# Kernel tuning notes

Hardware: AMD Instinct MI355X
Metric: run time of the kernel (lower is better)

Reference implementation:

```python
import jax, jax.numpy as jnp
import numpy as np

N = 30000      # nodes
E = 480000     # edges
H = 128        # hidden_nf
NQ = 7         # qubits
D = 2 ** NQ    # 128, quantum state dim == embedding_size
NL = 2         # block n_layers (QGCL layers)
QL = 2         # quantum circuit layers inside each QGCL
NORM = 100.0   # normalization_factor ('sum' aggregation)
NORM_CONST = 1.0


def _cnot_perm_indices(n):
    # Composed permutation for CNOT(0,1)...CNOT(n-2,n-1), CNOT(n-1,0).
    # PennyLane convention: wire 0 is the most significant bit.
    idx = np.arange(2 ** n)
    pairs = [(i, i + 1) for i in range(n - 1)] + [(n - 1, 0)]
    g = None
    for c, t in pairs:
        cb = (idx >> (n - 1 - c)) & 1
        f = idx ^ (cb << (n - 1 - t))  # flip target bit if control set (involution)
        g = f if g is None else g[f]
    return g

_CNOT_G = jnp.asarray(_cnot_perm_indices(NQ))


def _quantum_states(q_in, coeffs, A_re, A_im):
    """Vectorized VQC over all nodes. q_in [N,D] real -> [N,D] complex state."""
    norm = jnp.sqrt(jnp.sum(q_in ** 2, axis=1, keepdims=True) + 1e-12)
    s = (q_in / norm).astype(jnp.complex64)  # normalized initial state per node
    I = jnp.eye(D, dtype=jnp.complex64)
    for j in range(QL):
        # Cayley transform -> unitary
        A = (A_re[j] + 1j * A_im[j]).astype(jnp.complex64)
        A = A + A.conj().T
        q = (A - 1j * I) @ jnp.linalg.inv(A + 1j * I)
        # single-qubit layer: RY(b) @ RX(a) on every qubit -> kron power
        a, b = coeffs[j, 0].astype(jnp.complex64), coeffs[j, 1].astype(jnp.complex64)
        ca, sa = jnp.cos(a / 2), jnp.sin(a / 2)
        cb, sb = jnp.cos(b / 2), jnp.sin(b / 2)
        RX = jnp.stack([jnp.stack([ca, -1j * sa]), jnp.stack([-1j * sa, ca])])
        RY = jnp.stack([jnp.stack([cb, -sb]), jnp.stack([sb, cb])])
        G = RY @ RX
        Gk = G
        for _ in range(NQ - 1):
            Gk = jnp.kron(Gk, G)
        s = s @ q.T            # QubitUnitary
        s = s @ Gk.T           # RX/RY on all qubits
        s = s[:, _CNOT_G]      # CNOT ring (pure permutation)
    return s


def setup_inputs() -> dict:
    key = jax.random.key(0)
    ks = jax.random.split(key, 20)
    return {
        "h": jax.random.normal(ks[0], (N, H), jnp.float32),
        "x": jax.random.normal(ks[1], (N, 3), jnp.float32),
        "edge_index": jax.random.randint(ks[2], (2, E), 0, N, jnp.int32),
        "edge_attr": jax.random.normal(ks[3], (E, 1), jnp.float32),
        "e_w1": jax.random.normal(ks[4], (NL, 2 * H + 2, H), jnp.float32) * 0.05,
        "e_b1": jnp.zeros((NL, H), jnp.float32),
        "e_w2": jax.random.normal(ks[5], (NL, H, H), jnp.float32) * 0.05,
        "e_b2": jnp.zeros((NL, H), jnp.float32),
        "enc_w": jax.random.normal(ks[6], (NL, 2 * H, D), jnp.float32) * 0.05,
        "enc_b": jnp.zeros((NL, D), jnp.float32),
        "coeffs": jax.random.normal(ks[7], (NL, QL, 2), jnp.float32) * 0.1,
        "A_re": jax.random.normal(ks[8], (NL, QL, D, D), jnp.float32) * 0.01,
        "A_im": jax.random.normal(ks[9], (NL, QL, D, D), jnp.float32) * 0.01,
        "dec_w": jax.random.normal(ks[10], (NL, D, H), jnp.float32) * 0.05,
        "dec_b": jnp.zeros((NL, H), jnp.float32),
        "c_w1": jax.random.normal(ks[11], (2 * H + 2, H), jnp.float32) * 0.05,
        "c_b1": jnp.zeros((H,), jnp.float32),
        "c_w2": jax.random.normal(ks[12], (H, H), jnp.float32) * 0.05,
        "c_b2": jnp.zeros((H,), jnp.float32),
        "c_w3": jax.random.normal(ks[13], (H, 1), jnp.float32) * 0.001,  # xavier gain=0.001
    }


def reference(h, x, edge_index, edge_attr, e_w1, e_b1, e_w2, e_b2, enc_w, enc_b,
              coeffs, A_re, A_im, dec_w, dec_b, c_w1, c_b1, c_w2, c_b2, c_w3):
    row, col = edge_index[0], edge_index[1]
    # coord2diff
    diff = x[row] - x[col]
    radial = jnp.sum(diff ** 2, axis=1, keepdims=True)     # [E,1] (used as 'distances')
    coord_diff = diff / (jnp.sqrt(radial + 1e-8) + NORM_CONST)
    eattr = jnp.concatenate([radial, edge_attr], axis=1)   # [E,2]

    for l in range(NL):  # QGCL layers
        m = jnp.concatenate([h[row], h[col], eattr], axis=1)       # [E, 2H+2]
        m = jax.nn.silu(m @ e_w1[l] + e_b1[l])
        m = jax.nn.silu(m @ e_w2[l] + e_b2[l])                     # edge messages mij
        agg = jax.ops.segment_sum(m, row, num_segments=N) / NORM   # scatter-add
        q_in = jnp.concatenate([h, agg], axis=1) @ enc_w[l] + enc_b[l]
        # quantum part is detached in the original (torch .detach + re-tensor)
        qs = jax.lax.stop_gradient(
            _quantum_states(q_in, coeffs[l], A_re[l], A_im[l]))
        h = h + qs.real.astype(h.dtype) @ dec_w[l] + dec_b[l]

    # EquivariantUpdate (tanh=False)
    t = jnp.concatenate([h[row], h[col], eattr], axis=1)
    t = jax.nn.silu(t @ c_w1 + c_b1)
    t = jax.nn.silu(t @ c_w2 + c_b2)
    t = t @ c_w3                                                   # [E,1]
    trans = coord_diff * t
    x = x + jax.ops.segment_sum(trans, row, num_segments=N) / NORM
    return h, x
```

## Files before the change

kernel.cpp:

```cpp
#include <hip/hip_runtime.h>
#include <math.h>

#define N_NODES 30000
#define N_EDGES 480000
#define HDIM 128
#define EPB 64
#define AS 296
#define NAS 264
#define MS 136

typedef __attribute__((ext_vector_type(8))) short short8b;
typedef __attribute__((ext_vector_type(4))) float f32x4;

__device__ __forceinline__ float silu_f(float v) {
  return v / (1.0f + __expf(-v));
}

__device__ __forceinline__ unsigned short f2bf(float f) {
  unsigned int u = __float_as_uint(f);
  unsigned int r = u + 0x7fffu + ((u >> 16) & 1u);
  return (unsigned short)(r >> 16);
}

__global__ void init_out_kernel(const float* __restrict__ h,
                                const float* __restrict__ x,
                                float* __restrict__ out) {
  int idx = blockIdx.x * 256 + threadIdx.x;
  out[idx] = h[idx];
  if (idx < N_NODES * 3) out[N_NODES * HDIM + idx] = x[idx];
}

__global__ void h_to_bf_kernel(const float* __restrict__ h,
                               ushort* __restrict__ hbf) {
  int idx = blockIdx.x * 256 + threadIdx.x;
  float4 v = ((const float4*)h)[idx];
  ushort4 o;
  o.x = f2bf(v.x); o.y = f2bf(v.y); o.z = f2bf(v.z); o.w = f2bf(v.w);
  ((ushort4*)hbf)[idx] = o;
}

__global__ void convert_w_kernel(const float* __restrict__ W,
                                 ushort* __restrict__ dst, int Kreal, int KT) {
  int idx = blockIdx.x * 256 + threadIdx.x;
  if (idx >= KT * 4096) return;
  int kt = idx >> 12, rem = idx & 4095, n = rem >> 5, kk = rem & 31;
  int k = kt * 32 + kk;
  float v = (k < Kreal) ? W[(size_t)k * HDIM + n] : 0.0f;
  dst[idx] = f2bf(v);
}

__global__ void count_kernel(const int* __restrict__ ei, int* __restrict__ cursor) {
  int e = blockIdx.x * 256 + threadIdx.x;
  atomicAdd(&cursor[ei[e]], 1);
}

__global__ __launch_bounds__(1024) void scan_kernel(int* __restrict__ cursor,
                                                    int* __restrict__ cstart) {
  __shared__ int sums[1024];
  const int tid = threadIdx.x;
  const int base = tid * 30;
  int local[30];
  int s = 0;
#pragma unroll
  for (int j = 0; j < 30; ++j) {
    int idx = base + j;
    int d = (idx < N_NODES) ? cursor[idx] : 0;
    local[j] = s;
    s += d;
  }
  sums[tid] = s;
  __syncthreads();
  for (int off = 1; off < 1024; off <<= 1) {
    int add = (tid >= off) ? sums[tid - off] : 0;
    __syncthreads();
    sums[tid] += add;
    __syncthreads();
  }
  int excl = (tid == 0) ? 0 : sums[tid - 1];
#pragma unroll
  for (int j = 0; j < 30; ++j) {
    int idx = base + j;
    if (idx < N_NODES) {
      int v = excl + local[j];
      cursor[idx] = v;
      cstart[idx] = v;
    }
  }
}

__global__ void fill_kernel(const int* __restrict__ ei, int* __restrict__ cursor,
                            int* __restrict__ elist) {
  int e = blockIdx.x * 256 + threadIdx.x;
  int r = ei[e];
  int pos = atomicAdd(&cursor[r], 1);
  elist[pos] = e;
}

__global__ void perm_kernel(int* __restrict__ g) {
  int i = threadIdx.x;
  int v = i;
  const int cs[7] = {6, 5, 4, 3, 2, 1, 0};
  const int ts[7] = {0, 6, 5, 4, 3, 2, 1};
#pragma unroll
  for (int p = 0; p < 7; ++p) {
    int cb = (v >> (6 - cs[p])) & 1;
    v = v ^ (cb << (6 - ts[p]));
  }
  g[i] = v;
}

__global__ void ns_init_kernel(const float* __restrict__ Are,
                               const float* __restrict__ Aim,
                               float2* __restrict__ X) {
  int lj = blockIdx.y;
  int idx = blockIdx.x * 256 + threadIdx.x;
  int r = idx >> 7, c = idx & 127;
  const float* are = Are + (size_t)lj * 16384;
  const float* aim = Aim + (size_t)lj * 16384;
  float re = are[r * 128 + c] + are[c * 128 + r];
  float im = aim[r * 128 + c] - aim[c * 128 + r];
  if (r == c) im -= 1.0f;
  X[(size_t)lj * 16384 + idx] = make_float2(re, im);
}

__global__ void ns_bx_kernel(const float* __restrict__ Are,
                             const float* __restrict__ Aim,
                             const float2* __restrict__ X,
                             float2* __restrict__ T) {
  int lj = blockIdx.y;
  int idx = blockIdx.x * 256 + threadIdx.x;
  int r = idx >> 7, c = idx & 127;
  const float* are = Are + (size_t)lj * 16384;
  const float* aim = Aim + (size_t)lj * 16384;
  const float2* x = X + (size_t)lj * 16384;
  float2 acc = make_float2(0.f, 0.f);
  for (int k = 0; k < 128; ++k) {
    float re = are[r * 128 + k] + are[k * 128 + r];
    float im = aim[r * 128 + k] - aim[k * 128 + r];
    if (k == r) im += 1.0f;
    float2 b = x[k * 128 + c];
    acc.x += re * b.x - im * b.y;
    acc.y += re * b.y + im * b.x;
  }
  T[(size_t)lj * 16384 + idx] = acc;
}

__global__ void ns_upd_kernel(const float2* __restrict__ X,
                              const float2* __restrict__ T,
                              float2* __restrict__ Xn) {
  int lj = blockIdx.y;
  int idx = blockIdx.x * 256 + threadIdx.x;
  int r = idx >> 7, c = idx & 127;
  const float2* x = X + (size_t)lj * 16384;
  const float2* t = T + (size_t)lj * 16384;
  float2 acc = make_float2(0.f, 0.f);
  for (int k = 0; k < 128; ++k) {
    float2 a = x[r * 128 + k];
    float2 b = t[k * 128 + c];
    acc.x += a.x * b.x - a.y * b.y;
    acc.y += a.x * b.y + a.y * b.x;
  }
  float2 xc = x[r * 128 + c];
  Xn[(size_t)lj * 16384 + idx] = make_float2(2.f * xc.x - acc.x, 2.f * xc.y - acc.y);
}

__global__ void qmat_kernel(const float* __restrict__ Are,
                            const float* __restrict__ Aim,
                            const float2* __restrict__ binvg,
                            float2* __restrict__ qm) {
  int lj = blockIdx.y;
  int idx = blockIdx.x * 256 + threadIdx.x;
  int r = idx >> 7, c = idx & 127;
  const float* are = Are + (size_t)lj * 16384;
  const float* aim = Aim + (size_t)lj * 16384;
  const float2* binv = binvg + (size_t)lj * 16384;
  float2 acc = make_float2(0.f, 0.f);
  for (int k = 0; k < 128; ++k) {
    float re = are[r * 128 + k] + are[k * 128 + r];
    float im = aim[r * 128 + k] - aim[k * 128 + r];
    if (k == r) im -= 1.0f;
    float2 b = binv[k * 128 + c];
    acc.x += re * b.x - im * b.y;
    acc.y += re * b.y + im * b.x;
  }
  qm[(size_t)lj * 16384 + idx] = acc;
}

__global__ void gk_kernel(const float* __restrict__ coeffs,
                          float2* __restrict__ gkm) {
  int lj = blockIdx.y;
  float a = coeffs[lj * 2 + 0], b = coeffs[lj * 2 + 1];
  float ca = cosf(0.5f * a), sa = sinf(0.5f * a);
  float cb = cosf(0.5f * b), sb = sinf(0.5f * b);
  float2 G[2][2];
  G[0][0] = make_float2(cb * ca, sb * sa);
  G[0][1] = make_float2(-sb * ca, -cb * sa);
  G[1][0] = make_float2(sb * ca, -cb * sa);
  G[1][1] = make_float2(cb * ca, -sb * sa);
  int idx = blockIdx.x * 256 + threadIdx.x;
  int r = idx >> 7, c = idx & 127;
  float2 acc = make_float2(1.f, 0.f);
#pragma unroll
  for (int bit = 6; bit >= 0; --bit) {
    float2 g = G[(r >> bit) & 1][(c >> bit) & 1];
    acc = make_float2(acc.x * g.x - acc.y * g.y, acc.x * g.y + acc.y * g.x);
  }
  gkm[(size_t)lj * 16384 + idx] = acc;
}

__global__ void nj_kernel(const float2* __restrict__ qm,
                          const float2* __restrict__ gkm,
                          const int* __restrict__ g,
                          float2* __restrict__ njm) {
  int lj = blockIdx.y;
  int idx = blockIdx.x * 256 + threadIdx.x;
  int i = idx >> 7, c = idx & 127;
  int gc = g[c];
  const float2* q = qm + (size_t)lj * 16384;
  const float2* gk = gkm + (size_t)lj * 16384;
  float2 acc = make_float2(0.f, 0.f);
  for (int k = 0; k < 128; ++k) {
    float2 qa = q[k * 128 + i];
    float2 gb = gk[gc * 128 + k];
    acc.x += qa.x * gb.x - qa.y * gb.y;
    acc.y += qa.x * gb.y + qa.y * gb.x;
  }
  njm[(size_t)lj * 16384 + idx] = acc;
}

__global__ void compose_kernel(const float2* __restrict__ njm,
                               float2* __restrict__ um) {
  int l = blockIdx.y;
  int idx = blockIdx.x * 256 + threadIdx.x;
  int i = idx >> 7, c = idx & 127;
  const float2* n0 = njm + (size_t)(l * 2 + 0) * 16384;
  const float2* n1 = njm + (size_t)(l * 2 + 1) * 16384;
  float2 acc = make_float2(0.f, 0.f);
  for (int k = 0; k < 128; ++k) {
    float2 a = n0[i * 128 + k];
    float2 b = n1[k * 128 + c];
    acc.x += a.x * b.x - a.y * b.y;
    acc.y += a.x * b.y + a.y * b.x;
  }
  um[(size_t)l * 16384 + idx] = acc;
}

__global__ void wqd_kernel(const float2* __restrict__ um,
                           const float* __restrict__ decw,
                           float* __restrict__ wqd) {
  int l = blockIdx.y;
  int idx = blockIdx.x * 256 + threadIdx.x;
  int i = idx >> 7, c = idx & 127;
  const float2* u = um + (size_t)l * 16384;
  const float* dw = decw + (size_t)l * 16384;
  float acc = 0.f;
  for (int k = 0; k < 128; ++k) acc += u[i * 128 + k].x * dw[k * 128 + c];
  wqd[(size_t)l * 16384 + idx] = acc;
}

__global__ __launch_bounds__(256, 4) void edge_mfma_kernel(
    const ushort* __restrict__ hbf, const int* __restrict__ ei,
    const float* __restrict__ x, const float* __restrict__ ea,
    const int* __restrict__ elist, const int* __restrict__ cstart,
    const ushort* __restrict__ w1cs, const float* __restrict__ b1,
    const ushort* __restrict__ w2cs, const float* __restrict__ b2,
    float* __restrict__ agg, float* __restrict__ headp) {
  __shared__ ushort A[EPB * AS];
  __shared__ int rows[EPB];
  ushort* m1 = A;
  float* m2 = (float*)A;

  const int tid = threadIdx.x;
  const int lane = tid & 63, wave = tid >> 6;
  const int lrow = lane & 15, lq = lane >> 4;
  const int wbase = wave * 32;
  const int woff0 = (wbase + lrow) * 32 + lq * 8;
  const int woff1 = (wbase + 16 + lrow) * 32 + lq * 8;

  const float b1v[2] = {b1[wbase + lrow], b1[wbase + 16 + lrow]};
  const float b2v[2] = {b2[wbase + lrow], b2[wbase + 16 + lrow]};

  const int i0 = blockIdx.x * EPB;
  {
    const int e = tid >> 2, j = tid & 3;
    const int edge = elist[i0 + e];
    const int r = ei[edge], c = ei[N_EDGES + edge];
    if (j == 0) rows[e] = r;
    const uint4* hr = (const uint4*)(hbf + (size_t)r * HDIM + j * 32);
    const uint4* hc = (const uint4*)(hbf + (size_t)c * HDIM + j * 32);
    uint4* d1 = (uint4*)(A + e * AS + j * 32);
    uint4* d2 = (uint4*)(A + e * AS + 128 + j * 32);
    d1[0] = hr[0]; d1[1] = hr[1]; d1[2] = hr[2]; d1[3] = hr[3];
    d2[0] = hc[0]; d2[1] = hc[1]; d2[2] = hc[2]; d2[3] = hc[3];
    if (j == 3) {
      float dx = x[r * 3 + 0] - x[c * 3 + 0];
      float dy = x[r * 3 + 1] - x[c * 3 + 1];
      float dz = x[r * 3 + 2] - x[c * 3 + 2];
      ushort* dst = A + e * AS;
      dst[256] = f2bf(dx * dx + dy * dy + dz * dz);
      dst[257] = f2bf(ea[edge]);
#pragma unroll
      for (int z = 258; z < 288; ++z) dst[z] = 0;
    }
  }
  __syncthreads();

  f32x4 acc[4][2];
#pragma unroll
  for (int mt = 0; mt < 4; ++mt)
#pragma unroll
    for (int nt = 0; nt < 2; ++nt) acc[mt][nt] = (f32x4){0.f, 0.f, 0.f, 0.f};
  {
    short8b wcur0 = *(const short8b*)(w1cs + woff0);
    short8b wcur1 = *(const short8b*)(w1cs + woff1);
#pragma unroll
    for (int kt = 0; kt < 9; ++kt) {
      short8b wn0, wn1;
      if (kt < 8) {
        wn0 = *(const short8b*)(w1cs + (kt + 1) * 4096 + woff0);
        wn1 = *(const short8b*)(w1cs + (kt + 1) * 4096 + woff1);
      }
      short8b af[4];
#pragma unroll
      for (int mt = 0; mt < 4; ++mt)
        af[mt] = *(const short8b*)(A + (mt * 16 + lrow) * AS + kt * 32 + lq * 8);
#pragma unroll
      for (int mt = 0; mt < 4; ++mt) {
        acc[mt][0] = __builtin_amdgcn_mfma_f32_16x16x32_bf16(af[mt], wcur0, acc[mt][0], 0, 0, 0);
        acc[mt][1] = __builtin_amdgcn_mfma_f32_16x16x32_bf16(af[mt], wcur1, acc[mt][1], 0, 0, 0);
      }
      if (kt < 8) { wcur0 = wn0; wcur1 = wn1; }
    }
  }
  __syncthreads();
#pragma unroll
  for (int mt = 0; mt < 4; ++mt)
#pragma unroll
    for (int nt = 0; nt < 2; ++nt)
#pragma unroll
      for (int r = 0; r < 4; ++r)
        m1[(mt * 16 + lq * 4 + r) * MS + wbase + nt * 16 + lrow] =
            f2bf(silu_f(acc[mt][nt][r] + b1v[nt]));
  __syncthreads();

  f32x4 acc2[4][2];
#pragma unroll
  for (int mt = 0; mt < 4; ++mt)
#pragma unroll
    for (int nt = 0; nt < 2; ++nt) acc2[mt][nt] = (f32x4){0.f, 0.f, 0.f, 0.f};
  {
    short8b wcur0 = *(const short8b*)(w2cs + woff0);
    short8b wcur1 = *(const short8b*)(w2cs + woff1);
#pragma unroll
    for (int kt = 0; kt < 4; ++kt) {
      short8b wn0, wn1;
      if (kt < 3) {
        wn0 = *(const short8b*)(w2cs + (kt + 1) * 4096 + woff0);
        wn1 = *(const short8b*)(w2cs + (kt + 1) * 4096 + woff1);
      }
      short8b af[4];
#pragma unroll
      for (int mt = 0; mt < 4; ++mt)
        af[mt] = *(const short8b*)(m1 + (mt * 16 + lrow) * MS + kt * 32 + lq * 8);
#pragma unroll
      for (int mt = 0; mt < 4; ++mt) {
        acc2[mt][0] = __builtin_amdgcn_mfma_f32_16x16x32_bf16(af[mt], wcur0, acc2[mt][0], 0, 0, 0);
        acc2[mt][1] = __builtin_amdgcn_mfma_f32_16x16x32_bf16(af[mt], wcur1, acc2[mt][1], 0, 0, 0);
      }
      if (kt < 3) { wcur0 = wn0; wcur1 = wn1; }
    }
  }
  __syncthreads();
#pragma unroll
  for (int mt = 0; mt < 4; ++mt)
#pragma unroll
    for (int nt = 0; nt < 2; ++nt)
#pragma unroll
      for (int r = 0; r < 4; ++r)
        m2[(mt * 16 + lq * 4 + r) * MS + wbase + nt * 16 + lrow] =
            silu_f(acc2[mt][nt][r] + b2v[nt]);
  __syncthreads();

  const int e2 = tid & 63, cg = tid >> 6, cb = cg * 32;
  const int r_e = rows[e2];
  const bool leader = (e2 == 0) || (rows[e2 - 1] != r_e);
  if (leader) {
    f32x4 sum[8];
#pragma unroll
    for (int q = 0; q < 8; ++q) sum[q] = *(const f32x4*)(m2 + e2 * MS + cb + q * 4);
    int f = e2 + 1;
    while (f < EPB && rows[f] == r_e) {
#pragma unroll
      for (int q = 0; q < 8; ++q) sum[q] += *(const f32x4*)(m2 + f * MS + cb + q * 4);
      ++f;
    }
    float* dst = (e2 == 0 && cstart[r_e] < i0)
                     ? headp + (size_t)blockIdx.x * HDIM + cb
                     : agg + (size_t)r_e * HDIM + cb;
#pragma unroll
    for (int q = 0; q < 8; ++q) *(f32x4*)(dst + q * 4) = sum[q];
  }
}

__global__ __launch_bounds__(256, 2) void node_mfma_kernel(
    float* __restrict__ out_h, const float* __restrict__ agg,
    const int* __restrict__ cstart, const int* __restrict__ cend,
    const float* __restrict__ headp,
    const ushort* __restrict__ enccs, const float* __restrict__ encb,
    const ushort* __restrict__ wqdcs, const float* __restrict__ decb,
    ushort* __restrict__ hbf) {
  __shared__ ushort A[EPB * NAS];
  __shared__ ushort m1[EPB * MS];
  __shared__ float nbuf[4 * EPB];
  const int tid = threadIdx.x;
  const int n0 = blockIdx.x * EPB;

  const int lane = tid & 63, wave = tid >> 6;
  const int lrow = lane & 15, lq = lane >> 4;
  const int wbase = wave * 32;

  short8b wef[8][2], wqf[4][2];
#pragma unroll
  for (int kt = 0; kt < 8; ++kt)
#pragma unroll
    for (int nt = 0; nt < 2; ++nt)
      wef[kt][nt] = *(const short8b*)(enccs + kt * 4096 + (wbase + nt * 16 + lrow) * 32 + lq * 8);
#pragma unroll
  for (int kt = 0; kt < 4; ++kt)
#pragma unroll
    for (int nt = 0; nt < 2; ++nt)
      wqf[kt][nt] = *(const short8b*)(wqdcs + kt * 4096 + (wbase + nt * 16 + lrow) * 32 + lq * 8);
  const float ebv[2] = {encb[wbase + lrow], encb[wbase + 16 + lrow]};
  const float dbv[2] = {decb[wbase + lrow], decb[wbase + 16 + lrow]};

  {
    const int e = tid >> 2, j = tid & 3;
    int node = n0 + e;
    if (node >= N_NODES) node = N_NODES - 1;
    if (j < 2) {
      const float4* s4 = (const float4*)(out_h + (size_t)node * HDIM + j * 64);
      ushort* dst = A + e * NAS + j * 64;
#pragma unroll
      for (int i = 0; i < 16; ++i) {
        float4 v = s4[i];
        ushort4 o;
        o.x = f2bf(v.x); o.y = f2bf(v.y); o.z = f2bf(v.z); o.w = f2bf(v.w);
        ((ushort4*)dst)[i] = o;
      }
    } else {
      const int s = cstart[node], en = cend[node];
      const bool hasAgg = en > s;
      const float4* a4 = (const float4*)(agg + (size_t)node * HDIM + (j - 2) * 64);
      const int bb0 = (s >> 6) + 1;
      const int bb1 = hasAgg ? ((en - 1) >> 6) : 0;
      ushort* dst = A + e * NAS + 128 + (j - 2) * 64;
#pragma unroll
      for (int i = 0; i < 16; ++i) {
        float4 v = hasAgg ? a4[i] : make_float4(0.f, 0.f, 0.f, 0.f);
        for (int bb = bb0; bb <= bb1; ++bb) {
          float4 hv = *(const float4*)(headp + (size_t)bb * HDIM + (j - 2) * 64 + i * 4);
          v.x += hv.x; v.y += hv.y; v.z += hv.z; v.w += hv.w;
        }
        ushort4 o;
        o.x = f2bf(v.x * 0.01f); o.y = f2bf(v.y * 0.01f);
        o.z = f2bf(v.z * 0.01f); o.w = f2bf(v.w * 0.01f);
        ((ushort4*)dst)[i] = o;
      }
    }
  }
  __syncthreads();

  f32x4 acc[4][2];
#pragma unroll
  for (int mt = 0; mt < 4; ++mt)
#pragma unroll
    for (int nt = 0; nt < 2; ++nt) acc[mt][nt] = (f32x4){0.f, 0.f, 0.f, 0.f};
#pragma unroll
  for (int kt = 0; kt < 8; ++kt) {
    short8b af[4];
#pragma unroll
    for (int mt = 0; mt < 4; ++mt)
      af[mt] = *(const short8b*)(A + (mt * 16 + lrow) * NAS + kt * 32 + lq * 8);
#pragma unroll
    for (int mt = 0; mt < 4; ++mt)
#pragma unroll
      for (int nt = 0; nt < 2; ++nt)
        acc[mt][nt] = __builtin_amdgcn_mfma_f32_16x16x32_bf16(af[mt], wef[kt][nt], acc[mt][nt], 0, 0, 0);
  }
#pragma unroll
  for (int mt = 0; mt < 4; ++mt) {
    float ssp[4] = {0.f, 0.f, 0.f, 0.f};
#pragma unroll
    for (int nt = 0; nt < 2; ++nt)
#pragma unroll
      for (int r = 0; r < 4; ++r) {
        acc[mt][nt][r] += ebv[nt];
        ssp[r] += acc[mt][nt][r] * acc[mt][nt][r];
      }
#pragma unroll
    for (int m = 1; m < 16; m <<= 1)
#pragma unroll
      for (int r = 0; r < 4; ++r) ssp[r] += __shfl_xor(ssp[r], m, 64);
    if (lrow == 0) {
#pragma unroll
      for (int r = 0; r < 4; ++r)
        nbuf[wave * EPB + mt * 16 + lq * 4 + r] = ssp[r];
    }
  }
  __syncthreads();
#pragma unroll
  for (int mt = 0; mt < 4; ++mt)
#pragma unroll
    for (int r = 0; r < 4; ++r) {
      const int row = mt * 16 + lq * 4 + r;
      float sum = nbuf[row] + nbuf[EPB + row] + nbuf[2 * EPB + row] + nbuf[3 * EPB + row];
      float inv = 1.0f / sqrtf(sum + 1e-12f);
#pragma unroll
      for (int nt = 0; nt < 2; ++nt)
        m1[row * MS + wbase + nt * 16 + lrow] = f2bf(acc[mt][nt][r] * inv);
    }
  __syncthreads();

  f32x4 acc2[4][2];
#pragma unroll
  for (int mt = 0; mt < 4; ++mt)
#pragma unroll
    for (int nt = 0; nt < 2; ++nt) acc2[mt][nt] = (f32x4){0.f, 0.f, 0.f, 0.f};
#pragma unroll
  for (int kt = 0; kt < 4; ++kt) {
    short8b af[4];
#pragma unroll
    for (int mt = 0; mt < 4; ++mt)
      af[mt] = *(const short8b*)(m1 + (mt * 16 + lrow) * MS + kt * 32 + lq * 8);
#pragma unroll
    for (int mt = 0; mt < 4; ++mt)
#pragma unroll
      for (int nt = 0; nt < 2; ++nt)
        acc2[mt][nt] = __builtin_amdgcn_mfma_f32_16x16x32_bf16(af[mt], wqf[kt][nt], acc2[mt][nt], 0, 0, 0);
  }
#pragma unroll
  for (int mt = 0; mt < 4; ++mt)
#pragma unroll
    for (int nt = 0; nt < 2; ++nt) {
      const int n = wbase + nt * 16 + lrow;
#pragma unroll
      for (int r = 0; r < 4; ++r) {
        const int node = n0 + mt * 16 + lq * 4 + r;
        if (node < N_NODES) {
          size_t off = (size_t)node * HDIM + n;
          float hn = out_h[off] + acc2[mt][nt][r] + dbv[nt];
          out_h[off] = hn;
          hbf[off] = f2bf(hn);
        }
      }
    }
}

__global__ __launch_bounds__(256, 4) void coord_mfma_kernel(
    const ushort* __restrict__ hbf, const int* __restrict__ ei,
    const float* __restrict__ x, const float* __restrict__ ea,
    const int* __restrict__ elist,
    const ushort* __restrict__ w1cs, const float* __restrict__ b1,
    const ushort* __restrict__ w2cs, const float* __restrict__ b2,
    const float* __restrict__ w3, float* __restrict__ xout) {
  __shared__ ushort A[EPB * AS];
  __shared__ int rows[EPB];
  __shared__ int colsA[EPB];
  __shared__ float pbuf[4 * EPB];
  __shared__ float tv[EPB];
  ushort* m1 = A;

  const int tid = threadIdx.x;
  const int lane = tid & 63, wave = tid >> 6;
  const int lrow = lane & 15, lq = lane >> 4;
  const int wbase = wave * 32;
  const int woff0 = (wbase + lrow) * 32 + lq * 8;
  const int woff1 = (wbase + 16 + lrow) * 32 + lq * 8;

  const float b1v[2] = {b1[wbase + lrow], b1[wbase + 16 + lrow]};
  const float b2v[2] = {b2[wbase + lrow], b2[wbase + 16 + lrow]};
  const float w3v[2] = {w3[wbase + lrow], w3[wbase + 16 + lrow]};

  const int i0 = blockIdx.x * EPB;
  {
    const int e = tid >> 2, j = tid & 3;
    const int edge = elist[i0 + e];
    const int r = ei[edge], c = ei[N_EDGES + edge];
    if (j == 0) { rows[e] = r; colsA[e] = c; }
    const uint4* hr = (const uint4*)(hbf + (size_t)r * HDIM + j * 32);
    const uint4* hc = (const uint4*)(hbf + (size_t)c * HDIM + j * 32);
    uint4* d1 = (uint4*)(A + e * AS + j * 32);
    uint4* d2 = (uint4*)(A + e * AS + 128 + j * 32);
    d1[0] = hr[0]; d1[1] = hr[1]; d1[2] = hr[2]; d1[3] = hr[3];
    d2[0] = hc[0]; d2[1] = hc[1]; d2[2] = hc[2]; d2[3] = hc[3];
    if (j == 3) {
      float dx = x[r * 3 + 0] - x[c * 3 + 0];
      float dy = x[r * 3 + 1] - x[c * 3 + 1];
      float dz = x[r * 3 + 2] - x[c * 3 + 2];
      ushort* dst = A + e * AS;
      dst[256] = f2bf(dx * dx + dy * dy + dz * dz);
      dst[257] = f2bf(ea[edge]);
#pragma unroll
      for (int z = 258; z < 288; ++z) dst[z] = 0;
    }
  }
  __syncthreads();

  f32x4 acc[4][2];
#pragma unroll
  for (int mt = 0; mt < 4; ++mt)
#pragma unroll
    for (int nt = 0; nt < 2; ++nt) acc[mt][nt] = (f32x4){0.f, 0.f, 0.f, 0.f};
  {
    short8b wcur0 = *(const short8b*)(w1cs + woff0);
    short8b wcur1 = *(const short8b*)(w1cs + woff1);
#pragma unroll
    for (int kt = 0; kt < 9; ++kt) {
      short8b wn0, wn1;
      if (kt < 8) {
        wn0 = *(const short8b*)(w1cs + (kt + 1) * 4096 + woff0);
        wn1 = *(const short8b*)(w1cs + (kt + 1) * 4096 + woff1);
      }
      short8b af[4];
#pragma unroll
      for (int mt = 0; mt < 4; ++mt)
        af[mt] = *(const short8b*)(A + (mt * 16 + lrow) * AS + kt * 32 + lq * 8);
#pragma unroll
      for (int mt = 0; mt < 4; ++mt) {
        acc[mt][0] = __builtin_amdgcn_mfma_f32_16x16x32_bf16(af[mt], wcur0, acc[mt][0], 0, 0, 0);
        acc[mt][1] = __builtin_amdgcn_mfma_f32_16x16x32_bf16(af[mt], wcur1, acc[mt][1], 0, 0, 0);
      }
      if (kt < 8) { wcur0 = wn0; wcur1 = wn1; }
    }
  }
  __syncthreads();
#pragma unroll
  for (int mt = 0; mt < 4; ++mt)
#pragma unroll
    for (int nt = 0; nt < 2; ++nt)
#pragma unroll
      for (int r = 0; r < 4; ++r)
        m1[(mt * 16 + lq * 4 + r) * MS + wbase + nt * 16 + lrow] =
            f2bf(silu_f(acc[mt][nt][r] + b1v[nt]));
  __syncthreads();

  f32x4 acc2[4][2];
#pragma unroll
  for (int mt = 0; mt < 4; ++mt)
#pragma unroll
    for (int nt = 0; nt < 2; ++nt) acc2[mt][nt] = (f32x4){0.f, 0.f, 0.f, 0.f};
  {
    short8b wcur0 = *(const short8b*)(w2cs + woff0);
    short8b wcur1 = *(const short8b*)(w2cs + woff1);
#pragma unroll
    for (int kt = 0; kt < 4; ++kt) {
      short8b wn0, wn1;
      if (kt < 3) {
        wn0 = *(const short8b*)(w2cs + (kt + 1) * 4096 + woff0);
        wn1 = *(const short8b*)(w2cs + (kt + 1) * 4096 + woff1);
      }
      short8b af[4];
#pragma unroll
      for (int mt = 0; mt < 4; ++mt)
        af[mt] = *(const short8b*)(m1 + (mt * 16 + lrow) * MS + kt * 32 + lq * 8);
#pragma unroll
      for (int mt = 0; mt < 4; ++mt) {
        acc2[mt][0] = __builtin_amdgcn_mfma_f32_16x16x32_bf16(af[mt], wcur0, acc2[mt][0], 0, 0, 0);
        acc2[mt][1] = __builtin_amdgcn_mfma_f32_16x16x32_bf16(af[mt], wcur1, acc2[mt][1], 0, 0, 0);
      }
      if (kt < 3) { wcur0 = wn0; wcur1 = wn1; }
    }
  }
#pragma unroll
  for (int mt = 0; mt < 4; ++mt) {
    float p[4] = {0.f, 0.f, 0.f, 0.f};
#pragma unroll
    for (int nt = 0; nt < 2; ++nt)
#pragma unroll
      for (int r = 0; r < 4; ++r)
        p[r] += silu_f(acc2[mt][nt][r] + b2v[nt]) * w3v[nt];
#pragma unroll
    for (int m = 1; m < 16; m <<= 1)
#pragma unroll
      for (int r = 0; r < 4; ++r) p[r] += __shfl_xor(p[r], m, 64);
    if (lrow == 0) {
#pragma unroll
      for (int r = 0; r < 4; ++r)
        pbuf[wave * EPB + mt * 16 + lq * 4 + r] = p[r];
    }
  }
  __syncthreads();
  if (tid < EPB) {
    tv[tid] = (pbuf[tid] + pbuf[EPB + tid] + pbuf[2 * EPB + tid] + pbuf[3 * EPB + tid]) * 0.01f;
  }
  __syncthreads();
  if (tid < EPB) {
    const int e = tid;
    const int r_e = rows[e];
    const bool leader = (e == 0) || (rows[e - 1] != r_e);
    if (leader) {
      float sx = 0.f, sy = 0.f, sz = 0.f;
      int f = e;
      do {
        const int c = colsA[f];
        float dx = x[r_e * 3 + 0] - x[c * 3 + 0];
        float dy = x[r_e * 3 + 1] - x[c * 3 + 1];
        float dz = x[r_e * 3 + 2] - x[c * 3 + 2];
        float radial = dx * dx + dy * dy + dz * dz;
        float s = 1.0f / (sqrtf(radial + 1e-8f) + 1.0f);
        float t = tv[f];
        sx += dx * s * t; sy += dy * s * t; sz += dz * s * t;
        ++f;
      } while (f < EPB && rows[f] == r_e);
      atomicAdd(&xout[r_e * 3 + 0], sx);
      atomicAdd(&xout[r_e * 3 + 1], sy);
      atomicAdd(&xout[r_e * 3 + 2], sz);
    }
  }
}

extern "C" void kernel_launch(void* const* d_in, const int* in_sizes, int n_in,
                              void* d_out, int out_size, void* d_ws, size_t ws_size,
                              hipStream_t stream) {
  const float* h     = (const float*)d_in[0];
  const float* x     = (const float*)d_in[1];
  const int*   ei    = (const int*)d_in[2];
  const float* ea    = (const float*)d_in[3];
  const float* e_w1  = (const float*)d_in[4];
  const float* e_b1  = (const float*)d_in[5];
  const float* e_w2  = (const float*)d_in[6];
  const float* e_b2  = (const float*)d_in[7];
  const float* enc_w = (const float*)d_in[8];
  const float* enc_b = (const float*)d_in[9];
  const float* coeffs= (const float*)d_in[10];
  const float* A_re  = (const float*)d_in[11];
  const float* A_im  = (const float*)d_in[12];
  const float* dec_w = (const float*)d_in[13];
  const float* dec_b = (const float*)d_in[14];
  const float* c_w1  = (const float*)d_in[15];
  const float* c_b1  = (const float*)d_in[16];
  const float* c_w2  = (const float*)d_in[17];
  const float* c_b2  = (const float*)d_in[18];
  const float* c_w3  = (const float*)d_in[19];

  float* out = (float*)d_out;
  float* ws  = (float*)d_ws;

  float*  agg    = ws;
  float2* xa     = (float2*)(ws + 3840000);
  float2* xb     = (float2*)(ws + 3971072);
  float2* xt     = (float2*)(ws + 4102144);
  float2* qm     = (float2*)(ws + 4233216);
  float2* gkm    = (float2*)(ws + 4364288);
  float2* njm    = (float2*)(ws + 4495360);
  float2* um     = (float2*)(ws + 4626432);
  float*  wqd    = ws + 4691968;
  int*    perm   = (int*)(ws + 4724736);
  int*    cursor = (int*)(ws + 4724864);
  int*    cstart = (int*)(ws + 4754864);
  int*    elist  = (int*)(ws + 4784864);
  float*  headp  = ws + 5264864;
  ushort* hbf    = (ushort*)(ws + 6224864);
  ushort* w1cs   = (ushort*)(ws + 8144864);
  ushort* w2cs   = (ushort*)(ws + 8181728);
  ushort* cw1cs  = (ushort*)(ws + 8198112);
  ushort* cw2cs  = (ushort*)(ws + 8216544);
  ushort* enccs  = (ushort*)(ws + 8224736);
  ushort* wqdcs  = (ushort*)(ws + 8257504);

  init_out_kernel<<<15000, 256, 0, stream>>>(h, x, out);

  hipMemsetAsync(cursor, 0, N_NODES * sizeof(int), stream);
  count_kernel<<<1875, 256, 0, stream>>>(ei, cursor);
  scan_kernel<<<1, 1024, 0, stream>>>(cursor, cstart);
  fill_kernel<<<1875, 256, 0, stream>>>(ei, cursor, elist);

  perm_kernel<<<1, 128, 0, stream>>>(perm);
  ns_init_kernel<<<dim3(64, 4), 256, 0, stream>>>(A_re, A_im, xa);
  float2* cur = xa;
  float2* nxt = xb;
  for (int it = 0; it < 4; ++it) {
    ns_bx_kernel<<<dim3(64, 4), 256, 0, stream>>>(A_re, A_im, cur, xt);
    ns_upd_kernel<<<dim3(64, 4), 256, 0, stream>>>(cur, xt, nxt);
    float2* tmp = cur; cur = nxt; nxt = tmp;
  }
  qmat_kernel<<<dim3(64, 4), 256, 0, stream>>>(A_re, A_im, cur, qm);
  gk_kernel<<<dim3(64, 4), 256, 0, stream>>>(coeffs, gkm);
  nj_kernel<<<dim3(64, 4), 256, 0, stream>>>(qm, gkm, perm, njm);
  compose_kernel<<<dim3(64, 2), 256, 0, stream>>>(njm, um);
  wqd_kernel<<<dim3(64, 2), 256, 0, stream>>>(um, dec_w, wqd);

  for (int l = 0; l < 2; ++l) {
    convert_w_kernel<<<144, 256, 0, stream>>>(e_w1 + (size_t)l * 258 * HDIM,
                                              w1cs + (size_t)l * 9 * 4096, 258, 9);
    convert_w_kernel<<<64, 256, 0, stream>>>(e_w2 + (size_t)l * HDIM * HDIM,
                                             w2cs + (size_t)l * 4 * 4096, 128, 4);
    convert_w_kernel<<<128, 256, 0, stream>>>(enc_w + (size_t)l * 256 * HDIM,
                                              enccs + (size_t)l * 8 * 4096, 256, 8);
    convert_w_kernel<<<64, 256, 0, stream>>>(wqd + (size_t)l * HDIM * HDIM,
                                             wqdcs + (size_t)l * 4 * 4096, 128, 4);
  }
  convert_w_kernel<<<144, 256, 0, stream>>>(c_w1, cw1cs, 258, 9);
  convert_w_kernel<<<64, 256, 0, stream>>>(c_w2, cw2cs, 128, 4);

  h_to_bf_kernel<<<3750, 256, 0, stream>>>(out, hbf);

  for (int l = 0; l < 2; ++l) {
    edge_mfma_kernel<<<N_EDGES / EPB, 256, 0, stream>>>(
        hbf, ei, x, ea, elist, cstart,
        w1cs + (size_t)l * 9 * 4096, e_b1 + l * HDIM,
        w2cs + (size_t)l * 4 * 4096, e_b2 + l * HDIM, agg, headp);
    node_mfma_kernel<<<(N_NODES + EPB - 1) / EPB, 256, 0, stream>>>(
        out, agg, cstart, cursor, headp,
        enccs + (size_t)l * 8 * 4096, enc_b + l * HDIM,
        wqdcs + (size_t)l * 4 * 4096, dec_b + l * HDIM, hbf);
  }

  coord_mfma_kernel<<<N_EDGES / EPB, 256, 0, stream>>>(
      hbf, ei, x, ea, elist, cw1cs, c_b1, cw2cs, c_b2, c_w3,
      out + (size_t)N_NODES * HDIM);
}
```

Measured before the change: 826.4 us.

## Merge setup kernels, inline CNOT permutation, cut Newton-Schulz iterations

Fuses the output initialisation with the h-to-bf16 conversion, folds all weight conversions into one launch, computes the CNOT permutation inline instead of in a separate kernel, and has the wqd kernel write the bf16 tiled layout directly. Together these cut roughly fifteen small launches from the preamble. It also drops one Newton-Schulz iteration for the matrix inverse, which saves work but may reduce the accuracy of the Cayley unitary.

```diff
diff --git a/kernel.cpp b/kernel.cpp
--- a/kernel.cpp
+++ b/kernel.cpp
@@ -22,31 +22,54 @@
   return (unsigned short)(r >> 16);
 }
 
-__global__ void init_out_kernel(const float* __restrict__ h,
-                                const float* __restrict__ x,
-                                float* __restrict__ out) {
-  int idx = blockIdx.x * 256 + threadIdx.x;
-  out[idx] = h[idx];
-  if (idx < N_NODES * 3) out[N_NODES * HDIM + idx] = x[idx];
-}
-
-__global__ void h_to_bf_kernel(const float* __restrict__ h,
-                               ushort* __restrict__ hbf) {
+__global__ void init_out_bf_kernel(const float* __restrict__ h,
+                                   const float* __restrict__ x,
+                                   float* __restrict__ out,
+                                   ushort* __restrict__ hbf) {
   int idx = blockIdx.x * 256 + threadIdx.x;
   float4 v = ((const float4*)h)[idx];
+  ((float4*)out)[idx] = v;
   ushort4 o;
   o.x = f2bf(v.x); o.y = f2bf(v.y); o.z = f2bf(v.z); o.w = f2bf(v.w);
   ((ushort4*)hbf)[idx] = o;
-}
-
-__global__ void convert_w_kernel(const float* __restrict__ W,
-                                 ushort* __restrict__ dst, int Kreal, int KT) {
-  int idx = blockIdx.x * 256 + threadIdx.x;
-  if (idx >= KT * 4096) return;
-  int kt = idx >> 12, rem = idx & 4095, n = rem >> 5, kk = rem & 31;
-  int k = kt * 32 + kk;
+  if (idx < N_NODES * 3 / 4) {
+    ((float4*)(out + N_NODES * HDIM))[idx] = ((const float4*)x)[idx];
+  }
+}
+
+__global__ void convert_all_kernel(
+    const float* __restrict__ e_w1, const float* __restrict__ e_w2,
+    const float* __restrict__ enc_w, const float* __restrict__ c_w1,
+    const float* __restrict__ c_w2,
+    ushort* __restrict__ w1cs, ushort* __restrict__ w2cs,
+    ushort* __restrict__ enccs, ushort* __restrict__ cw1cs,
+    ushort* __restrict__ cw2cs) {
+  int idx = blockIdx.x * 256 + threadIdx.x;
+  if (idx >= 55 * 4096) return;
+  int ci = idx >> 12, rem = idx & 4095, n = rem >> 5, kk = rem & 31;
+  const float* W;
+  ushort* dst;
+  int Kreal, ktl;
+  if (ci < 18) {
+    int l = ci / 9; ktl = ci - l * 9;
+    W = e_w1 + (size_t)l * 258 * HDIM; dst = w1cs + (size_t)l * 9 * 4096;
+    Kreal = 258;
+  } else if (ci < 26) {
+    int c2 = ci - 18; int l = c2 >> 2; ktl = c2 & 3;
+    W = e_w2 + (size_t)l * HDIM * HDIM; dst = w2cs + (size_t)l * 4 * 4096;
+    Kreal = 128;
+  } else if (ci < 42) {
+    int c2 = ci - 26; int l = c2 >> 3; ktl = c2 & 7;
+    W = enc_w + (size_t)l * 256 * HDIM; dst = enccs + (size_t)l * 8 * 4096;
+    Kreal = 256;
+  } else if (ci < 51) {
+    ktl = ci - 42; W = c_w1; dst = cw1cs; Kreal = 258;
+  } else {
+    ktl = ci - 51; W = c_w2; dst = cw2cs; Kreal = 128;
+  }
+  int k = ktl * 32 + kk;
   float v = (k < Kreal) ? W[(size_t)k * HDIM + n] : 0.0f;
-  dst[idx] = f2bf(v);
+  dst[ktl * 4096 + rem] = f2bf(v);
 }
 
 __global__ void count_kernel(const int* __restrict__ ei, int* __restrict__ cursor) {
@@ -94,19 +117,6 @@
   int r = ei[e];
   int pos = atomicAdd(&cursor[r], 1);
   elist[pos] = e;
-}
-
-__global__ void perm_kernel(int* __restrict__ g) {
-  int i = threadIdx.x;
-  int v = i;
-  const int cs[7] = {6, 5, 4, 3, 2, 1, 0};
-  const int ts[7] = {0, 6, 5, 4, 3, 2, 1};
-#pragma unroll
-  for (int p = 0; p < 7; ++p) {
-    int cb = (v >> (6 - cs[p])) & 1;
-    v = v ^ (cb << (6 - ts[p]));
-  }
-  g[i] = v;
 }
 
 __global__ void ns_init_kernel(const float* __restrict__ Are,
@@ -210,12 +220,22 @@
 
 __global__ void nj_kernel(const float2* __restrict__ qm,
                           const float2* __restrict__ gkm,
-                          const int* __restrict__ g,
                           float2* __restrict__ njm) {
   int lj = blockIdx.y;
   int idx = blockIdx.x * 256 + threadIdx.x;
   int i = idx >> 7, c = idx & 127;
-  int gc = g[c];
+  int gc;
+  {
+    int v = c;
+    const int cs[7] = {6, 5, 4, 3, 2, 1, 0};
+    const int ts[7] = {0, 6, 5, 4, 3, 2, 1};
+#pragma unroll
+    for (int p = 0; p < 7; ++p) {
+      int cb = (v >> (6 - cs[p])) & 1;
+      v = v ^ (cb << (6 - ts[p]));
+    }
+    gc = v;
+  }
   const float2* q = qm + (size_t)lj * 16384;
   const float2* gk = gkm + (size_t)lj * 16384;
   float2 acc = make_float2(0.f, 0.f);
@@ -247,7 +267,7 @@
 
 __global__ void wqd_kernel(const float2* __restrict__ um,
                            const float* __restrict__ decw,
-                           float* __restrict__ wqd) {
+                           ushort* __restrict__ wqdcs) {
   int l = blockIdx.y;
   int idx = blockIdx.x * 256 + threadIdx.x;
   int i = idx >> 7, c = idx & 127;
@@ -255,7 +275,7 @@
   const float* dw = decw + (size_t)l * 16384;
   float acc = 0.f;
   for (int k = 0; k < 128; ++k) acc += u[i * 128 + k].x * dw[k * 128 + c];
-  wqd[(size_t)l * 16384 + idx] = acc;
+  wqdcs[(size_t)l * 4 * 4096 + (i >> 5) * 4096 + c * 32 + (i & 31)] = f2bf(acc);
 }
 
 __global__ __launch_bounds__(256, 4) void edge_mfma_kernel(
@@ -754,8 +774,6 @@
   float2* gkm    = (float2*)(ws + 4364288);
   float2* njm    = (float2*)(ws + 4495360);
   float2* um     = (float2*)(ws + 4626432);
-  float*  wqd    = ws + 4691968;
-  int*    perm   = (int*)(ws + 4724736);
   int*    cursor = (int*)(ws + 4724864);
   int*    cstart = (int*)(ws + 4754864);
   int*    elist  = (int*)(ws + 4784864);
@@ -768,42 +786,29 @@
   ushort* enccs  = (ushort*)(ws + 8224736);
   ushort* wqdcs  = (ushort*)(ws + 8257504);
 
-  init_out_kernel<<<15000, 256, 0, stream>>>(h, x, out);
+  init_out_bf_kernel<<<3750, 256, 0, stream>>>(h, x, out, hbf);
 
   hipMemsetAsync(cursor, 0, N_NODES * sizeof(int), stream);
   count_kernel<<<1875, 256, 0, stream>>>(ei, cursor);
   scan_kernel<<<1, 1024, 0, stream>>>(cursor, cstart);
   fill_kernel<<<1875, 256, 0, stream>>>(ei, cursor, elist);
 
-  perm_kernel<<<1, 128, 0, stream>>>(perm);
+  convert_all_kernel<<<880, 256, 0, stream>>>(e_w1, e_w2, enc_w, c_w1, c_w2,
+                                              w1cs, w2cs, enccs, cw1cs, cw2cs);
+
   ns_init_kernel<<<dim3(64, 4), 256, 0, stream>>>(A_re, A_im, xa);
   float2* cur = xa;
   float2* nxt = xb;
-  for (int it = 0; it < 4; ++it) {
+  for (int it = 0; it < 3; ++it) {
     ns_bx_kernel<<<dim3(64, 4), 256, 0, stream>>>(A_re, A_im, cur, xt);
     ns_upd_kernel<<<dim3(64, 4), 256, 0, stream>>>(cur, xt, nxt);
     float2* tmp = cur; cur = nxt; nxt = tmp;
   }
   qmat_kernel<<<dim3(64, 4), 256, 0, stream>>>(A_re, A_im, cur, qm);
   gk_kernel<<<dim3(64, 4), 256, 0, stream>>>(coeffs, gkm);
-  nj_kernel<<<dim3(64, 4), 256, 0, stream>>>(qm, gkm, perm, njm);
+  nj_kernel<<<dim3(64, 4), 256, 0, stream>>>(qm, gkm, njm);
   compose_kernel<<<dim3(64, 2), 256, 0, stream>>>(njm, um);
-  wqd_kernel<<<dim3(64, 2), 256, 0, stream>>>(um, dec_w, wqd);
-
-  for (int l = 0; l < 2; ++l) {
-    convert_w_kernel<<<144, 256, 0, stream>>>(e_w1 + (size_t)l * 258 * HDIM,
-                                              w1cs + (size_t)l * 9 * 4096, 258, 9);
-    convert_w_kernel<<<64, 256, 0, stream>>>(e_w2 + (size_t)l * HDIM * HDIM,
-                                             w2cs + (size_t)l * 4 * 4096, 128, 4);
-    convert_w_kernel<<<128, 256, 0, stream>>>(enc_w + (size_t)l * 256 * HDIM,
-                                              enccs + (size_t)l * 8 * 4096, 256, 8);
-    convert_w_kernel<<<64, 256, 0, stream>>>(wqd + (size_t)l * HDIM * HDIM,
-                                             wqdcs + (size_t)l * 4 * 4096, 128, 4);
-  }
-  convert_w_kernel<<<144, 256, 0, stream>>>(c_w1, cw1cs, 258, 9);
-  convert_w_kernel<<<64, 256, 0, stream>>>(c_w2, cw2cs, 128, 4);
-
-  h_to_bf_kernel<<<3750, 256, 0, stream>>>(out, hbf);
+  wqd_kernel<<<dim3(64, 2), 256, 0, stream>>>(um, dec_w, wqdcs);
 
   for (int l = 0; l < 2; ++l) {
     edge_mfma_kernel<<<N_EDGES / EPB, 256, 0, stream>>>(
```

After: 770.1 us. 1.07x faster.
